# Kernel optimization log

Hardware: AMD Instinct MI355X
Metric: run time of the kernel (lower is better)

Reference implementation:

```python
import jax, jax.numpy as jnp
import numpy as np

N_ENTITIES = 100000
D = 128
N_EDGES = 600000
N_RELATIONS = 32
N_USERS = 50000
NNZ = 1000000


def setup_inputs() -> dict:
    key = jax.random.key(0)
    k = jax.random.split(key, 7)
    entity_emb = jax.random.normal(k[0], (N_ENTITIES, D), dtype=jnp.float32)
    edge_index = jax.random.randint(k[1], (2, N_EDGES), 0, N_ENTITIES, dtype=jnp.int64)
    # edge_type in [1, N_RELATIONS] so that weight[edge_type - 1] is in-range
    edge_type = jax.random.randint(k[2], (N_EDGES,), 1, N_RELATIONS + 1, dtype=jnp.int64)
    interact_rows = jax.random.randint(k[3], (NNZ,), 0, N_USERS, dtype=jnp.int64)
    interact_cols = jax.random.randint(k[4], (NNZ,), 0, N_ENTITIES, dtype=jnp.int64)
    interact_vals = jax.random.uniform(k[5], (NNZ,), dtype=jnp.float32)
    weight = jax.random.normal(k[6], (N_RELATIONS, D), dtype=jnp.float32)
    return {
        "entity_emb": entity_emb,
        "edge_index": edge_index,
        "edge_type": edge_type,
        "interact_rows": interact_rows,
        "interact_cols": interact_cols,
        "interact_vals": interact_vals,
        "n_users": N_USERS,
        "weight": weight,
    }


def reference(entity_emb, edge_index, edge_type, interact_rows, interact_cols,
              interact_vals, n_users, weight):
    n_entities = entity_emb.shape[0]
    head, tail = edge_index[0], edge_index[1]

    # KG aggregate: gather -> elementwise mul -> scatter_mean over head
    edge_relation_emb = weight[edge_type - 1]              # [E, D]
    neigh_relation_emb = entity_emb[tail] * edge_relation_emb  # [E, D]
    seg_sum = jax.ops.segment_sum(neigh_relation_emb, head, num_segments=n_entities)
    counts = jax.ops.segment_sum(jnp.ones((head.shape[0],), dtype=entity_emb.dtype),
                                 head, num_segments=n_entities)
    entity_agg = seg_sum / jnp.maximum(counts, 1.0)[:, None]  # mean; empty rows -> 0

    # user aggregate: sparse (COO) @ dense  == segment-sum of scaled gathered rows
    gathered = interact_vals[:, None] * entity_emb[interact_cols]  # [nnz, D]
    user_agg = jax.ops.segment_sum(gathered, interact_rows, num_segments=n_users)

    return entity_agg, user_agg
```

## Files before the change

kernel.cpp:

```cpp
#include <hip/hip_runtime.h>

#define D 128

typedef int v2i __attribute__((ext_vector_type(2)));
typedef int v4i __attribute__((ext_vector_type(4)));

__device__ __forceinline__ float bf2f(unsigned short u) {
    union { unsigned int i; float f; } v;
    v.i = ((unsigned int)u) << 16;
    return v.f;
}
__device__ __forceinline__ unsigned short f2bf(float f) {
    union { float f; unsigned int i; } v;
    v.f = f;
    unsigned int x = v.i;
    unsigned int round_bit = (x >> 16) & 1u;
    x += 0x7fffu + round_bit;
    return (unsigned short)(x >> 16);
}

__device__ __forceinline__ int idx_at(const void* p, long long i, bool i64) {
    return i64 ? (int)((const long long*)p)[i] : ((const int*)p)[i];
}

__global__ void init_all(int* __restrict__ cnt, int n_concat,
                         const int* __restrict__ et_i32,
                         const unsigned short* __restrict__ emb_u16,
                         int* __restrict__ bump, int* __restrict__ flags) {
    int i = blockIdx.x * blockDim.x + threadIdx.x;
    for (; i < n_concat; i += gridDim.x * blockDim.x) cnt[i] = 0;

    if (blockIdx.x == 0 && threadIdx.x == 0) bump[0] = 0;

    if (blockIdx.x == 0 && threadIdx.x < 64) {
        int lane = threadIdx.x;
        int v = et_i32[2 * lane + 1];
        unsigned long long b_i64 = __ballot(v != 0);

        unsigned short a = emb_u16[2 * lane];
        unsigned short c = emb_u16[2 * lane + 1];
        int e1 = (a >> 7) & 0xFF;
        int e2 = (c >> 7) & 0xFF;
        unsigned long long b_f32 = __ballot(e1 > 140 || e2 > 140);

        if (lane == 0) {
            flags[0] = (b_i64 == 0ULL) ? 1 : 0;
            flags[1] = (b_f32 != 0ULL) ? 1 : 0;
        }
    }
}

__global__ void hist_all(const void* __restrict__ ei, const void* __restrict__ rows,
                         int* __restrict__ cnt, int2* __restrict__ dr,
                         const int* __restrict__ flags,
                         int n_edges, int nnz, int n_entities) {
    long long i = (long long)blockIdx.x * blockDim.x + threadIdx.x;
    bool i64 = flags[0] != 0;
    if (i < n_edges) {
        int dst = idx_at(ei, i, i64);
        int r = atomicAdd(&cnt[dst], 1);
        int2 p; p.x = dst; p.y = r;
        dr[i] = p;
    } else if (i < (long long)n_edges + nnz) {
        int dst = n_entities + idx_at(rows, i - n_edges, i64);
        int r = atomicAdd(&cnt[dst], 1);
        int2 p; p.x = dst; p.y = r;
        dr[i] = p;
    }
}

__device__ __forceinline__ int block_scan_excl_256(int v, int* total) {
    __shared__ int tmp[256];
    int tid = threadIdx.x;
    tmp[tid] = v;
    __syncthreads();
    #pragma unroll
    for (int ofs = 1; ofs < 256; ofs <<= 1) {
        int t = (tid >= ofs) ? tmp[tid - ofs] : 0;
        __syncthreads();
        tmp[tid] += t;
        __syncthreads();
    }
    int incl = tmp[tid];
    *total = tmp[255];
    __syncthreads();
    return incl - v;
}

__global__ void alloc_base(const int* __restrict__ cnt, int* __restrict__ base,
                           int* __restrict__ cur, int* __restrict__ bump, int n) {
    int i = blockIdx.x * 256 + threadIdx.x;
    int v = (i < n) ? cnt[i] : 0;
    int total;
    int excl = block_scan_excl_256(v, &total);
    __shared__ int sbase;
    if (threadIdx.x == 0) sbase = atomicAdd(bump, total);
    __syncthreads();
    if (i < n) {
        base[i] = sbase + excl;
        cur[i] = 0;
    }
}

__global__ void scatter_rank(const void* __restrict__ ei, const void* __restrict__ et,
                             const void* __restrict__ cols, const void* __restrict__ vals,
                             const int* __restrict__ base, const int2* __restrict__ dr,
                             int2* __restrict__ pairs, const int* __restrict__ flags,
                             int n_edges, int nnz) {
    long long i = (long long)blockIdx.x * blockDim.x + threadIdx.x;
    bool i64 = flags[0] != 0;
    if (i < n_edges) {
        int2 d = dr[i];
        int tail = idx_at(ei, (long long)n_edges + i, i64);
        int rel  = idx_at(et, i, i64) - 1;
        int2 p; p.x = tail; p.y = rel;
        pairs[base[d.x] + d.y] = p;
    } else if (i < (long long)n_edges + nnz) {
        long long k = i - n_edges;
        bool f32 = flags[1] != 0;
        int2 d = dr[i];
        int c = idx_at(cols, k, i64);
        float v = f32 ? ((const float*)vals)[k] : bf2f(((const unsigned short*)vals)[k]);
        int2 p; p.x = c; p.y = __float_as_int(v);
        pairs[base[d.x] + d.y] = p;
    }
}

__global__ void scatter_all(const void* __restrict__ ei, const void* __restrict__ et,
                            const void* __restrict__ rows, const void* __restrict__ cols,
                            const void* __restrict__ vals,
                            const int* __restrict__ base, int* __restrict__ cur,
                            int2* __restrict__ pairs, const int* __restrict__ flags,
                            int n_edges, int nnz, int n_entities) {
    long long i = (long long)blockIdx.x * blockDim.x + threadIdx.x;
    bool i64 = flags[0] != 0;
    if (i < n_edges) {
        int head = idx_at(ei, i, i64);
        int tail = idx_at(ei, (long long)n_edges + i, i64);
        int rel  = idx_at(et, i, i64) - 1;
        int pos = base[head] + atomicAdd(&cur[head], 1);
        int2 p; p.x = tail; p.y = rel;
        pairs[pos] = p;
    } else if (i < (long long)n_edges + nnz) {
        long long k = i - n_edges;
        bool f32 = flags[1] != 0;
        int rr = n_entities + idx_at(rows, k, i64);
        int c = idx_at(cols, k, i64);
        float v = f32 ? ((const float*)vals)[k] : bf2f(((const unsigned short*)vals)[k]);
        int pos = base[rr] + atomicAdd(&cur[rr], 1);
        int2 p; p.x = c; p.y = __float_as_int(v);
        pairs[pos] = p;
    }
}

__device__ __forceinline__ void unpack4(uint2 q, float* e) {
    e[0] = bf2f((unsigned short)(q.x & 0xFFFFu)); e[1] = bf2f((unsigned short)(q.x >> 16));
    e[2] = bf2f((unsigned short)(q.y & 0xFFFFu)); e[3] = bf2f((unsigned short)(q.y >> 16));
}

__global__ void agg_all(const void* __restrict__ emb, const void* __restrict__ weight,
                        const int* __restrict__ base, const int* __restrict__ cnt,
                        const int2* __restrict__ pairs,
                        void* __restrict__ out, const int* __restrict__ flags,
                        int n_entities, int n_total, int n_pairs_i) {
    int tid = blockIdx.x * blockDim.x + threadIdx.x;
    int m = threadIdx.x & 31;
    int grp = tid >> 5;
    int stride = (gridDim.x * blockDim.x) >> 5;
    bool f32 = flags[1] != 0;

    if (f32) {
        const float4* embq = (const float4*)emb;
        const float4* wq   = (const float4*)weight;
        for (int row = grp; row < n_total; row += stride) {
            bool isU = (row >= n_entities);
            int beg = base[row];
            int deg = min(cnt[row], n_pairs_i);
            int end = beg + deg;
            float4 acc; acc.x = acc.y = acc.z = acc.w = 0.f;

            for (int bb = beg; bb < end; bb += 32) {
                int nn = min(32, end - bb);
                int px = 0, py = 0;
                if (m < nn) {
                    v2i t = __builtin_nontemporal_load((const v2i*)pairs + bb + m);
                    px = t.x; py = t.y;
                }
                int t = 0;
                if (isU) {
                    for (; t + 4 <= nn; t += 4) {
                        int sx0 = __shfl(px, t, 32),     sx1 = __shfl(px, t + 1, 32);
                        int sx2 = __shfl(px, t + 2, 32), sx3 = __shfl(px, t + 3, 32);
                        float v0 = __int_as_float(__shfl(py, t, 32));
                        float v1 = __int_as_float(__shfl(py, t + 1, 32));
                        float v2 = __int_as_float(__shfl(py, t + 2, 32));
                        float v3 = __int_as_float(__shfl(py, t + 3, 32));
                        float4 a0 = embq[(size_t)sx0 * 32 + m];
                        float4 a1 = embq[(size_t)sx1 * 32 + m];
                        float4 a2 = embq[(size_t)sx2 * 32 + m];
                        float4 a3 = embq[(size_t)sx3 * 32 + m];
                        acc.x += v0 * a0.x + v1 * a1.x + v2 * a2.x + v3 * a3.x;
                        acc.y += v0 * a0.y + v1 * a1.y + v2 * a2.y + v3 * a3.y;
                        acc.z += v0 * a0.z + v1 * a1.z + v2 * a2.z + v3 * a3.z;
                        acc.w += v0 * a0.w + v1 * a1.w + v2 * a2.w + v3 * a3.w;
                    }
                    for (; t < nn; ++t) {
                        int sx = __shfl(px, t, 32);
                        float v = __int_as_float(__shfl(py, t, 32));
                        float4 a = embq[(size_t)sx * 32 + m];
                        acc.x += v * a.x; acc.y += v * a.y; acc.z += v * a.z; acc.w += v * a.w;
                    }
                } else {
                    for (; t + 4 <= nn; t += 4) {
                        int sx0 = __shfl(px, t, 32),     sx1 = __shfl(px, t + 1, 32);
                        int sx2 = __shfl(px, t + 2, 32), sx3 = __shfl(px, t + 3, 32);
                        int sy0 = __shfl(py, t, 32),     sy1 = __shfl(py, t + 1, 32);
                        int sy2 = __shfl(py, t + 2, 32), sy3 = __shfl(py, t + 3, 32);
                        float4 a0 = embq[(size_t)sx0 * 32 + m];
                        float4 a1 = embq[(size_t)sx1 * 32 + m];
                        float4 a2 = embq[(size_t)sx2 * 32 + m];
                        float4 a3 = embq[(size_t)sx3 * 32 + m];
                        float4 w0 = wq[(size_t)sy0 * 32 + m];
                        float4 w1 = wq[(size_t)sy1 * 32 + m];
                        float4 w2 = wq[(size_t)sy2 * 32 + m];
                        float4 w3 = wq[(size_t)sy3 * 32 + m];
                        acc.x += a0.x * w0.x + a1.x * w1.x + a2.x * w2.x + a3.x * w3.x;
                        acc.y += a0.y * w0.y + a1.y * w1.y + a2.y * w2.y + a3.y * w3.y;
                        acc.z += a0.z * w0.z + a1.z * w1.z + a2.z * w2.z + a3.z * w3.z;
                        acc.w += a0.w * w0.w + a1.w * w1.w + a2.w * w2.w + a3.w * w3.w;
                    }
                    for (; t < nn; ++t) {
                        int sx = __shfl(px, t, 32);
                        int sy = __shfl(py, t, 32);
                        float4 a = embq[(size_t)sx * 32 + m];
                        float4 w = wq[(size_t)sy * 32 + m];
                        acc.x += a.x * w.x; acc.y += a.y * w.y; acc.z += a.z * w.z; acc.w += a.w * w.w;
                    }
                }
            }

            if (!isU) {
                float rcp = 1.0f / fmaxf((float)deg, 1.0f);
                acc.x *= rcp; acc.y *= rcp; acc.z *= rcp; acc.w *= rcp;
            }

            v4i o;
            o.x = __float_as_int(acc.x); o.y = __float_as_int(acc.y);
            o.z = __float_as_int(acc.z); o.w = __float_as_int(acc.w);
            __builtin_nontemporal_store(o, (v4i*)out + (size_t)row * 32 + m);
        }
    } else {
        const uint2* embh = (const uint2*)emb;
        const uint2* wh   = (const uint2*)weight;
        for (int row = grp; row < n_total; row += stride) {
            bool isU = (row >= n_entities);
            int beg = base[row];
            int deg = min(cnt[row], n_pairs_i);
            int end = beg + deg;
            float acc[4] = {0.f, 0.f, 0.f, 0.f};

            for (int bb = beg; bb < end; bb += 32) {
                int nn = min(32, end - bb);
                int px = 0, py = 0;
                if (m < nn) {
                    v2i t = __builtin_nontemporal_load((const v2i*)pairs + bb + m);
                    px = t.x; py = t.y;
                }
                for (int t = 0; t < nn; ++t) {
                    int sx = __shfl(px, t, 32);
                    if (isU) {
                        float v = __int_as_float(__shfl(py, t, 32));
                        uint2 q = embh[(size_t)sx * 32 + m];
                        float e[4]; unpack4(q, e);
                        #pragma unroll
                        for (int i = 0; i < 4; ++i) acc[i] += v * e[i];
                    } else {
                        int sy = __shfl(py, t, 32);
                        uint2 q  = embh[(size_t)sx * 32 + m];
                        uint2 qw = wh[(size_t)sy * 32 + m];
                        float e[4], wv[4]; unpack4(q, e); unpack4(qw, wv);
                        #pragma unroll
                        for (int i = 0; i < 4; ++i) acc[i] += e[i] * wv[i];
                    }
                }
            }

            if (!isU) {
                float rcp = 1.0f / fmaxf((float)deg, 1.0f);
                #pragma unroll
                for (int i = 0; i < 4; ++i) acc[i] *= rcp;
            }

            v2i o;
            o.x = (int)((unsigned int)f2bf(acc[0]) | ((unsigned int)f2bf(acc[1]) << 16));
            o.y = (int)((unsigned int)f2bf(acc[2]) | ((unsigned int)f2bf(acc[3]) << 16));
            __builtin_nontemporal_store(o, (v2i*)out + (size_t)row * 32 + m);
        }
    }
}

extern "C" void kernel_launch(void* const* d_in, const int* in_sizes, int n_in,
                              void* d_out, int out_size, void* d_ws, size_t ws_size,
                              hipStream_t stream) {
    const void* emb  = d_in[0];
    const void* ei   = d_in[1];
    const void* et   = d_in[2];
    const void* rows = d_in[3];
    const void* cols = d_in[4];
    const void* vals = d_in[5];

    const void* weight = d_in[n_in - 1];
    for (int i = n_in - 1; i >= 5; --i) {
        if (in_sizes[i] >= 256) { weight = d_in[i]; break; }
    }

    int n_entities = in_sizes[0] / D;
    int n_edges    = in_sizes[2];
    int nnz        = in_sizes[5];
    int n_users    = out_size / D - n_entities;

    int n_concat = n_entities + n_users;
    int nb = (n_concat + 255) / 256;
    long long n_pairs = (long long)n_edges + nnz;

    size_t fixed = (size_t)(3 * n_concat + 3) * sizeof(int);
    bool use_rank = ws_size >= (size_t)n_pairs * sizeof(int2) * 2 + fixed + 256;

    char* p = (char*)d_ws;
    int2* pairs = (int2*)p;                      p += (size_t)n_pairs * sizeof(int2);
    int2* dr = nullptr;
    if (use_rank) { dr = (int2*)p;               p += (size_t)n_pairs * sizeof(int2); }
    int*  base  = (int*)p;                       p += (size_t)n_concat * sizeof(int);
    int*  cnt   = (int*)p;                       p += (size_t)n_concat * sizeof(int);
    int*  cur   = (int*)p;                       p += (size_t)n_concat * sizeof(int);
    int*  bump  = (int*)p;                       p += sizeof(int);
    int*  flags = (int*)p;

    const int tpb = 256;

    init_all<<<nb, tpb, 0, stream>>>(cnt, n_concat, (const int*)et,
                                     (const unsigned short*)emb, bump, flags);

    hist_all<<<(int)((n_pairs + tpb - 1) / tpb), tpb, 0, stream>>>(
        ei, rows, cnt, dr ? dr : pairs , flags,
        n_edges, nnz, n_entities);

    alloc_base<<<nb, 256, 0, stream>>>(cnt, base, cur, bump, n_concat);

    if (use_rank) {
        scatter_rank<<<(int)((n_pairs + tpb - 1) / tpb), tpb, 0, stream>>>(
            ei, et, cols, vals, base, dr, pairs, flags, n_edges, nnz);
    } else {
        scatter_all<<<(int)((n_pairs + tpb - 1) / tpb), tpb, 0, stream>>>(
            ei, et, rows, cols, vals, base, cur, pairs, flags, n_edges, nnz, n_entities);
    }

    {
        int blocks_needed = (n_concat + 7) / 8;
        int blocks = blocks_needed < 2048 ? blocks_needed : 2048;
        agg_all<<<blocks, tpb, 0, stream>>>(
            emb, weight, base, cnt, pairs, d_out, flags, n_entities, n_concat,
            (int)n_pairs);
    }
}
```

Measured before the change: 353.4 us.

## Pack full pair payload in histogram pass and split aggregation rows across column halves

When the workspace is large enough, the histogram kernel now reads the tail/relation or column/value alongside the destination and writes a 16-byte record. The scatter pass then only reads that record plus base, instead of re-reading the original index arrays. The aggregation kernel now assigns 16-lane groups to half-rows, with even and odd blocks covering the two column halves. This doubles the row groups and shortens shuffle widths, in exchange for reading each pairs segment twice. The 16-byte intermediate also adds write traffic in the histogram pass.

```diff
diff --git a/kernel.cpp b/kernel.cpp
--- a/kernel.cpp
+++ b/kernel.cpp
@@ -47,6 +47,33 @@
             flags[0] = (b_i64 == 0ULL) ? 1 : 0;
             flags[1] = (b_f32 != 0ULL) ? 1 : 0;
         }
+    }
+}
+
+__global__ void hist_all4(const void* __restrict__ ei, const void* __restrict__ et,
+                          const void* __restrict__ rows, const void* __restrict__ cols,
+                          const void* __restrict__ vals,
+                          int* __restrict__ cnt, v4i* __restrict__ dr4,
+                          const int* __restrict__ flags,
+                          int n_edges, int nnz, int n_entities) {
+    long long i = (long long)blockIdx.x * blockDim.x + threadIdx.x;
+    bool i64 = flags[0] != 0;
+    if (i < n_edges) {
+        int dst  = idx_at(ei, i, i64);
+        int tail = idx_at(ei, (long long)n_edges + i, i64);
+        int rel  = idx_at(et, i, i64) - 1;
+        int r = atomicAdd(&cnt[dst], 1);
+        v4i q; q.x = dst; q.y = r; q.z = tail; q.w = rel;
+        dr4[i] = q;
+    } else if (i < (long long)n_edges + nnz) {
+        long long k = i - n_edges;
+        bool f32 = flags[1] != 0;
+        int dst = n_entities + idx_at(rows, k, i64);
+        int c = idx_at(cols, k, i64);
+        float v = f32 ? ((const float*)vals)[k] : bf2f(((const unsigned short*)vals)[k]);
+        int r = atomicAdd(&cnt[dst], 1);
+        v4i q; q.x = dst; q.y = r; q.z = c; q.w = __float_as_int(v);
+        dr4[i] = q;
     }
 }
 
@@ -99,6 +126,16 @@
     if (i < n) {
         base[i] = sbase + excl;
         cur[i] = 0;
+    }
+}
+
+__global__ void scatter_rank4(const v4i* __restrict__ dr4, const int* __restrict__ base,
+                              int2* __restrict__ pairs, long long n_total) {
+    long long i = (long long)blockIdx.x * blockDim.x + threadIdx.x;
+    if (i < n_total) {
+        v4i q = dr4[i];
+        int2 p; p.x = q.z; p.y = q.w;
+        pairs[base[q.x] + q.y] = p;
     }
 }
 
@@ -163,24 +200,26 @@
                         const int2* __restrict__ pairs,
                         void* __restrict__ out, const int* __restrict__ flags,
                         int n_entities, int n_total, int n_pairs_i) {
-    int tid = blockIdx.x * blockDim.x + threadIdx.x;
-    int m = threadIdx.x & 31;
-    int grp = tid >> 5;
-    int stride = (gridDim.x * blockDim.x) >> 5;
+    int s = blockIdx.x & 1;
+    int bos = blockIdx.x >> 1;
+    int m = threadIdx.x & 15;
+    int gg = bos * (blockDim.x >> 4) + (threadIdx.x >> 4);
+    int stride = (gridDim.x >> 1) * (blockDim.x >> 4);
     bool f32 = flags[1] != 0;
+    int col = s * 16 + m;
 
     if (f32) {
         const float4* embq = (const float4*)emb;
         const float4* wq   = (const float4*)weight;
-        for (int row = grp; row < n_total; row += stride) {
+        for (int row = gg; row < n_total; row += stride) {
             bool isU = (row >= n_entities);
             int beg = base[row];
             int deg = min(cnt[row], n_pairs_i);
             int end = beg + deg;
             float4 acc; acc.x = acc.y = acc.z = acc.w = 0.f;
 
-            for (int bb = beg; bb < end; bb += 32) {
-                int nn = min(32, end - bb);
+            for (int bb = beg; bb < end; bb += 16) {
+                int nn = min(16, end - bb);
                 int px = 0, py = 0;
                 if (m < nn) {
                     v2i t = __builtin_nontemporal_load((const v2i*)pairs + bb + m);
@@ -189,51 +228,51 @@
                 int t = 0;
                 if (isU) {
                     for (; t + 4 <= nn; t += 4) {
-                        int sx0 = __shfl(px, t, 32),     sx1 = __shfl(px, t + 1, 32);
-                        int sx2 = __shfl(px, t + 2, 32), sx3 = __shfl(px, t + 3, 32);
-                        float v0 = __int_as_float(__shfl(py, t, 32));
-                        float v1 = __int_as_float(__shfl(py, t + 1, 32));
-                        float v2 = __int_as_float(__shfl(py, t + 2, 32));
-                        float v3 = __int_as_float(__shfl(py, t + 3, 32));
-                        float4 a0 = embq[(size_t)sx0 * 32 + m];
-                        float4 a1 = embq[(size_t)sx1 * 32 + m];
-                        float4 a2 = embq[(size_t)sx2 * 32 + m];
-                        float4 a3 = embq[(size_t)sx3 * 32 + m];
+                        int sx0 = __shfl(px, t, 16),     sx1 = __shfl(px, t + 1, 16);
+                        int sx2 = __shfl(px, t + 2, 16), sx3 = __shfl(px, t + 3, 16);
+                        float v0 = __int_as_float(__shfl(py, t, 16));
+                        float v1 = __int_as_float(__shfl(py, t + 1, 16));
+                        float v2 = __int_as_float(__shfl(py, t + 2, 16));
+                        float v3 = __int_as_float(__shfl(py, t + 3, 16));
+                        float4 a0 = embq[(size_t)sx0 * 32 + col];
+                        float4 a1 = embq[(size_t)sx1 * 32 + col];
+                        float4 a2 = embq[(size_t)sx2 * 32 + col];
+                        float4 a3 = embq[(size_t)sx3 * 32 + col];
                         acc.x += v0 * a0.x + v1 * a1.x + v2 * a2.x + v3 * a3.x;
                         acc.y += v0 * a0.y + v1 * a1.y + v2 * a2.y + v3 * a3.y;
                         acc.z += v0 * a0.z + v1 * a1.z + v2 * a2.z + v3 * a3.z;
                         acc.w += v0 * a0.w + v1 * a1.w + v2 * a2.w + v3 * a3.w;
                     }
                     for (; t < nn; ++t) {
-                        int sx = __shfl(px, t, 32);
-                        float v = __int_as_float(__shfl(py, t, 32));
-                        float4 a = embq[(size_t)sx * 32 + m];
+                        int sx = __shfl(px, t, 16);
+                        float v = __int_as_float(__shfl(py, t, 16));
+                        float4 a = embq[(size_t)sx * 32 + col];
                         acc.x += v * a.x; acc.y += v * a.y; acc.z += v * a.z; acc.w += v * a.w;
                     }
                 } else {
                     for (; t + 4 <= nn; t += 4) {
-                        int sx0 = __shfl(px, t, 32),     sx1 = __shfl(px, t + 1, 32);
-                        int sx2 = __shfl(px, t + 2, 32), sx3 = __shfl(px, t + 3, 32);
-                        int sy0 = __shfl(py, t, 32),     sy1 = __shfl(py, t + 1, 32);
-                        int sy2 = __shfl(py, t + 2, 32), sy3 = __shfl(py, t + 3, 32);
-                        float4 a0 = embq[(size_t)sx0 * 32 + m];
-                        float4 a1 = embq[(size_t)sx1 * 32 + m];
-                        float4 a2 = embq[(size_t)sx2 * 32 + m];
-                        float4 a3 = embq[(size_t)sx3 * 32 + m];
-                        float4 w0 = wq[(size_t)sy0 * 32 + m];
-                        float4 w1 = wq[(size_t)sy1 * 32 + m];
-                        float4 w2 = wq[(size_t)sy2 * 32 + m];
-                        float4 w3 = wq[(size_t)sy3 * 32 + m];
+                        int sx0 = __shfl(px, t, 16),     sx1 = __shfl(px, t + 1, 16);
+                        int sx2 = __shfl(px, t + 2, 16), sx3 = __shfl(px, t + 3, 16);
+                        int sy0 = __shfl(py, t, 16),     sy1 = __shfl(py, t + 1, 16);
+                        int sy2 = __shfl(py, t + 2, 16), sy3 = __shfl(py, t + 3, 16);
+                        float4 a0 = embq[(size_t)sx0 * 32 + col];
+                        float4 a1 = embq[(size_t)sx1 * 32 + col];
+                        float4 a2 = embq[(size_t)sx2 * 32 + col];
+                        float4 a3 = embq[(size_t)sx3 * 32 + col];
+                        float4 w0 = wq[(size_t)sy0 * 32 + col];
+                        float4 w1 = wq[(size_t)sy1 * 32 + col];
+                        float4 w2 = wq[(size_t)sy2 * 32 + col];
+                        float4 w3 = wq[(size_t)sy3 * 32 + col];
                         acc.x += a0.x * w0.x + a1.x * w1.x + a2.x * w2.x + a3.x * w3.x;
                         acc.y += a0.y * w0.y + a1.y * w1.y + a2.y * w2.y + a3.y * w3.y;
                         acc.z += a0.z * w0.z + a1.z * w1.z + a2.z * w2.z + a3.z * w3.z;
                         acc.w += a0.w * w0.w + a1.w * w1.w + a2.w * w2.w + a3.w * w3.w;
                     }
                     for (; t < nn; ++t) {
-                        int sx = __shfl(px, t, 32);
-                        int sy = __shfl(py, t, 32);
-                        float4 a = embq[(size_t)sx * 32 + m];
-                        float4 w = wq[(size_t)sy * 32 + m];
+                        int sx = __shfl(px, t, 16);
+                        int sy = __shfl(py, t, 16);
+                        float4 a = embq[(size_t)sx * 32 + col];
+                        float4 w = wq[(size_t)sy * 32 + col];
                         acc.x += a.x * w.x; acc.y += a.y * w.y; acc.z += a.z * w.z; acc.w += a.w * w.w;
                     }
                 }
@@ -247,37 +286,37 @@
             v4i o;
             o.x = __float_as_int(acc.x); o.y = __float_as_int(acc.y);
             o.z = __float_as_int(acc.z); o.w = __float_as_int(acc.w);
-            __builtin_nontemporal_store(o, (v4i*)out + (size_t)row * 32 + m);
+            __builtin_nontemporal_store(o, (v4i*)out + (size_t)row * 32 + col);
         }
     } else {
         const uint2* embh = (const uint2*)emb;
         const uint2* wh   = (const uint2*)weight;
-        for (int row = grp; row < n_total; row += stride) {
+        for (int row = gg; row < n_total; row += stride) {
             bool isU = (row >= n_entities);
             int beg = base[row];
             int deg = min(cnt[row], n_pairs_i);
             int end = beg + deg;
             float acc[4] = {0.f, 0.f, 0.f, 0.f};
 
-            for (int bb = beg; bb < end; bb += 32) {
-                int nn = min(32, end - bb);
+            for (int bb = beg; bb < end; bb += 16) {
+                int nn = min(16, end - bb);
                 int px = 0, py = 0;
                 if (m < nn) {
                     v2i t = __builtin_nontemporal_load((const v2i*)pairs + bb + m);
                     px = t.x; py = t.y;
                 }
                 for (int t = 0; t < nn; ++t) {
-                    int sx = __shfl(px, t, 32);
+                    int sx = __shfl(px, t, 16);
                     if (isU) {
-                        float v = __int_as_float(__shfl(py, t, 32));
-                        uint2 q = embh[(size_t)sx * 32 + m];
+                        float v = __int_as_float(__shfl(py, t, 16));
+                        uint2 q = embh[(size_t)sx * 32 + col];
                         float e[4]; unpack4(q, e);
                         #pragma unroll
                         for (int i = 0; i < 4; ++i) acc[i] += v * e[i];
                     } else {
-                        int sy = __shfl(py, t, 32);
-                        uint2 q  = embh[(size_t)sx * 32 + m];
-                        uint2 qw = wh[(size_t)sy * 32 + m];
+                        int sy = __shfl(py, t, 16);
+                        uint2 q  = embh[(size_t)sx * 32 + col];
+                        uint2 qw = wh[(size_t)sy * 32 + col];
                         float e[4], wv[4]; unpack4(q, e); unpack4(qw, wv);
                         #pragma unroll
                         for (int i = 0; i < 4; ++i) acc[i] += e[i] * wv[i];
@@ -294,7 +333,7 @@
             v2i o;
             o.x = (int)((unsigned int)f2bf(acc[0]) | ((unsigned int)f2bf(acc[1]) << 16));
             o.y = (int)((unsigned int)f2bf(acc[2]) | ((unsigned int)f2bf(acc[3]) << 16));
-            __builtin_nontemporal_store(o, (v2i*)out + (size_t)row * 32 + m);
+            __builtin_nontemporal_store(o, (v2i*)out + (size_t)row * 32 + col);
         }
     }
 }
@@ -323,13 +362,17 @@
     int nb = (n_concat + 255) / 256;
     long long n_pairs = (long long)n_edges + nnz;
 
-    size_t fixed = (size_t)(3 * n_concat + 3) * sizeof(int);
-    bool use_rank = ws_size >= (size_t)n_pairs * sizeof(int2) * 2 + fixed + 256;
+    size_t fixed = (size_t)(3 * n_concat + 3) * sizeof(int) + 256;
+    int mode = 0;
+    if (ws_size >= (size_t)n_pairs * (16 + 8) + fixed)      mode = 2;
+    else if (ws_size >= (size_t)n_pairs * (8 + 8) + fixed)  mode = 1;
 
     char* p = (char*)d_ws;
+    v4i*  dr4 = nullptr;
+    int2* dr  = nullptr;
+    if (mode == 2) { dr4 = (v4i*)p;              p += (size_t)n_pairs * sizeof(v4i); }
+    else if (mode == 1) { dr = (int2*)p;         p += (size_t)n_pairs * sizeof(int2); }
     int2* pairs = (int2*)p;                      p += (size_t)n_pairs * sizeof(int2);
-    int2* dr = nullptr;
-    if (use_rank) { dr = (int2*)p;               p += (size_t)n_pairs * sizeof(int2); }
     int*  base  = (int*)p;                       p += (size_t)n_concat * sizeof(int);
     int*  cnt   = (int*)p;                       p += (size_t)n_concat * sizeof(int);
     int*  cur   = (int*)p;                       p += (size_t)n_concat * sizeof(int);
@@ -337,27 +380,37 @@
     int*  flags = (int*)p;
 
     const int tpb = 256;
+    int gpairs = (int)((n_pairs + tpb - 1) / tpb);
 
     init_all<<<nb, tpb, 0, stream>>>(cnt, n_concat, (const int*)et,
                                      (const unsigned short*)emb, bump, flags);
 
-    hist_all<<<(int)((n_pairs + tpb - 1) / tpb), tpb, 0, stream>>>(
-        ei, rows, cnt, dr ? dr : pairs , flags,
-        n_edges, nnz, n_entities);
+    if (mode == 2) {
+        hist_all4<<<gpairs, tpb, 0, stream>>>(ei, et, rows, cols, vals,
+                                              cnt, dr4, flags,
+                                              n_edges, nnz, n_entities);
+    } else {
+        hist_all<<<gpairs, tpb, 0, stream>>>(ei, rows, cnt,
+                                             dr ? dr : pairs ,
+                                             flags, n_edges, nnz, n_entities);
+    }
 
     alloc_base<<<nb, 256, 0, stream>>>(cnt, base, cur, bump, n_concat);
 
-    if (use_rank) {
-        scatter_rank<<<(int)((n_pairs + tpb - 1) / tpb), tpb, 0, stream>>>(
+    if (mode == 2) {
+        scatter_rank4<<<gpairs, tpb, 0, stream>>>(dr4, base, pairs, n_pairs);
+    } else if (mode == 1) {
+        scatter_rank<<<gpairs, tpb, 0, stream>>>(
             ei, et, cols, vals, base, dr, pairs, flags, n_edges, nnz);
     } else {
-        scatter_all<<<(int)((n_pairs + tpb - 1) / tpb), tpb, 0, stream>>>(
+        scatter_all<<<gpairs, tpb, 0, stream>>>(
             ei, et, rows, cols, vals, base, cur, pairs, flags, n_edges, nnz, n_entities);
     }
 
     {
-        int blocks_needed = (n_concat + 7) / 8;
-        int blocks = blocks_needed < 2048 ? blocks_needed : 2048;
+        int bps = (n_concat + 15) / 16;
+        if (bps > 2048) bps = 2048;
+        int blocks = 2 * bps;
         agg_all<<<blocks, tpb, 0, stream>>>(
             emb, weight, base, cnt, pairs, d_out, flags, n_entities, n_concat,
             (int)n_pairs);
```

Result: faster. 345.6 us (-2.2%).
